# Performance work log

Hardware: AMD Instinct MI355X
Metric: run time of the kernel (lower is better)

The kernel has to match this reference:

```python
import jax, jax.numpy as jnp
import numpy as np

N, K, G = 4096, 4096, 128  # out_features, in_features, groupsize


def setup_inputs() -> dict:
    key = jax.random.key(0)
    k1, k2, k3, k4 = jax.random.split(key, 4)
    input = jax.random.normal(k1, (1, 2048, K), dtype=jnp.float32)
    # packed int4 weights: each byte holds two 4-bit codes (high nibble = even k, low = odd k)
    weight_packed = jax.random.randint(k2, (N, K // 2), 0, 256, dtype=jnp.int32)
    scales = jax.random.uniform(k3, (K // G, N), dtype=jnp.float32) * 0.02 + 1e-3
    zeros = jax.random.normal(k4, (K // G, N), dtype=jnp.float32) * 0.05
    scales_and_zeros = jnp.stack([scales, zeros], axis=-1)  # (K//G, N, 2)
    return {"input": input, "weight_packed": weight_packed,
            "scales_and_zeros": scales_and_zeros, "groupsize": G}


def reference(input, weight_packed, scales_and_zeros, groupsize):
    n, k_half = weight_packed.shape
    k = 2 * k_half
    g = k // groupsize
    # unpack two int4 codes per byte: high nibble first (even k index), then low nibble
    hi = (weight_packed >> 4) & 0xF
    lo = weight_packed & 0xF
    q = jnp.stack([hi, lo], axis=-1).reshape(n, k)  # (N, K), codes in [0,15]
    scales = scales_and_zeros[..., 0].T  # (N, G)
    zeros = scales_and_zeros[..., 1].T   # (N, G)
    # group-wise affine dequant: w = (q - 8) * scale + zero
    qg = q.reshape(n, g, groupsize).astype(jnp.float32)
    w = (qg - 8.0) * scales[:, :, None] + zeros[:, :, None]  # (N, G, gs)
    w = w.reshape(n, k)
    # out[..., n] = sum_k input[..., k] * w[n, k]
    return jnp.einsum('bsk,nk->bsn', input, w)
```

## Files before the change

### kernel.cpp

```cpp
#include <hip/hip_runtime.h>
#include <hip/hip_bf16.h>


using bf16x8 = __attribute__((ext_vector_type(8))) short;
using f32x16 = __attribute__((ext_vector_type(16))) float;

#define KK 4096
#define NN 4096
#define NT (KK / 64)

static __device__ __forceinline__ short f2bf(float f) {
    __hip_bfloat16 h = __float2bfloat16(f);
    return __builtin_bit_cast(short, h);
}

#define GLDS16(gptr, lptr) __builtin_amdgcn_global_load_lds( \
    (const __attribute__((address_space(1))) void*)(gptr),   \
    (__attribute__((address_space(3))) void*)(lptr), 16, 0, 0)

#define MFMA32 __builtin_amdgcn_mfma_f32_32x32x16_bf16

__global__ __launch_bounds__(256) void dequant_w(
    const int* __restrict__ W, const float* __restrict__ SZ,
    short* __restrict__ Wd)
{
    const int idx = blockIdx.x * 256 + threadIdx.x;
    const int n   = idx >> 9;
    const int q4  = idx & 511;
    const int kh0 = q4 << 2;
    const int g   = kh0 >> 6;
    const float2 sz = *(const float2*)(SZ + ((size_t)g * NN + n) * 2);
    const float scale = sz.x;
    const float zs    = sz.y - 8.0f * sz.x;
    int4 p = *(const int4*)(W + (size_t)n * (KK / 2) + kh0);
    int vals[4] = {p.x, p.y, p.z, p.w};
    bf16x8 r;
    #pragma unroll
    for (int j = 0; j < 4; ++j) {
        int v = vals[j];
        r[2 * j]     = f2bf((float)((v >> 4) & 0xF) * scale + zs);
        r[2 * j + 1] = f2bf((float)(v & 0xF) * scale + zs);
    }
    *(bf16x8*)&Wd[(size_t)n * KK + (kh0 << 1)] = r;
}

__global__ __launch_bounds__(256) void cvt_a(
    const float* __restrict__ A, short* __restrict__ Ab)
{
    const int idx = blockIdx.x * 256 + threadIdx.x;
    const float4* s = (const float4*)(A + (size_t)idx * 8);
    float4 u = s[0], v = s[1];
    bf16x8 r;
    r[0] = f2bf(u.x); r[1] = f2bf(u.y); r[2] = f2bf(u.z); r[3] = f2bf(u.w);
    r[4] = f2bf(v.x); r[5] = f2bf(v.y); r[6] = f2bf(v.z); r[7] = f2bf(v.w);
    *(bf16x8*)&Ab[(size_t)idx * 8] = r;
}

__global__ __launch_bounds__(512, 2) void gemm32(
    const short* __restrict__ Ab, const short* __restrict__ Bb,
    float* __restrict__ C)
{
    __shared__ short sA[3 * 256 * 64];
    __shared__ short sB[3 * 128 * 64];

    const int tid  = threadIdx.x;
    const int lane = tid & 63;
    const int wave = tid >> 6;
    const int wm   = wave >> 1;
    const int wn   = wave & 1;
    const int bm   = blockIdx.y * 256;
    const int bn   = blockIdx.x * 128;

    const int sl = lane >> 3;
    const int sc = (lane & 7) ^ sl;
    const short* aSt = Ab + (size_t)(bm + wave * 32 + sl) * KK + sc * 8;
    const short* bSt = Bb + (size_t)(bn + wave * 16 + sl) * KK + sc * 8;

    const int l31 = lane & 31;
    const int lx  = lane >> 5;
    const int l7  = lane & 7;
    const int px0 = ((0 + lx) ^ l7) * 8;
    const int px1 = ((2 + lx) ^ l7) * 8;
    const int px2 = ((4 + lx) ^ l7) * 8;
    const int px3 = ((6 + lx) ^ l7) * 8;
    const int aRd = (wm * 64 + l31) * 64;
    const int bRd = (wn * 64 + l31) * 64;

    f32x16 acc00 = {}, acc01 = {}, acc10 = {}, acc11 = {};

    #pragma unroll
    for (int l = 0; l < 4; ++l)
        GLDS16(aSt + (size_t)l * 8 * KK,      &sA[(wave * 32 + l * 8) * 64]);
    #pragma unroll
    for (int l = 0; l < 2; ++l)
        GLDS16(bSt + (size_t)l * 8 * KK,      &sB[(wave * 16 + l * 8) * 64]);
    #pragma unroll
    for (int l = 0; l < 4; ++l)
        GLDS16(aSt + (size_t)l * 8 * KK + 64, &sA[16384 + (wave * 32 + l * 8) * 64]);
    #pragma unroll
    for (int l = 0; l < 2; ++l)
        GLDS16(bSt + (size_t)l * 8 * KK + 64, &sB[8192 + (wave * 16 + l * 8) * 64]);
    asm volatile("s_waitcnt vmcnt(6)" ::: "memory");
    __builtin_amdgcn_s_barrier();

    int cur = 0;
    for (int t = 0; t < NT; ++t) {
        const int nxt = (cur == 0) ? 2 : cur - 1;
        const short* sAc = &sA[cur * 16384];
        const short* sBc = &sB[cur * 8192];
        short* sAn = &sA[nxt * 16384];
        short* sBn = &sB[nxt * 8192];
        const bool st = (t + 2 < NT);
        const int gk = (t + 2) * 64;

        {
            bf16x8 a00 = *(const bf16x8*)&sAc[aRd + px0];
            bf16x8 a01 = *(const bf16x8*)&sAc[aRd + px1];
            bf16x8 a10 = *(const bf16x8*)&sAc[aRd + 2048 + px0];
            bf16x8 a11 = *(const bf16x8*)&sAc[aRd + 2048 + px1];
            bf16x8 b00 = *(const bf16x8*)&sBc[bRd + px0];
            bf16x8 b01 = *(const bf16x8*)&sBc[bRd + px1];
            bf16x8 b10 = *(const bf16x8*)&sBc[bRd + 2048 + px0];
            bf16x8 b11 = *(const bf16x8*)&sBc[bRd + 2048 + px1];
            if (st) {
                GLDS16(aSt + (size_t)0 * 8 * KK + gk, sAn + (wave * 32 + 0) * 64);
                GLDS16(aSt + (size_t)1 * 8 * KK + gk, sAn + (wave * 32 + 8) * 64);
                GLDS16(bSt + (size_t)0 * 8 * KK + gk, sBn + (wave * 16 + 0) * 64);
            }
            __builtin_amdgcn_s_barrier();
            asm volatile("s_waitcnt lgkmcnt(0)" ::: "memory");
            __builtin_amdgcn_s_setprio(1);
            acc00 = MFMA32(a00, b00, acc00, 0, 0, 0);
            acc00 = MFMA32(a01, b01, acc00, 0, 0, 0);
            acc01 = MFMA32(a00, b10, acc01, 0, 0, 0);
            acc01 = MFMA32(a01, b11, acc01, 0, 0, 0);
            acc10 = MFMA32(a10, b00, acc10, 0, 0, 0);
            acc10 = MFMA32(a11, b01, acc10, 0, 0, 0);
            acc11 = MFMA32(a10, b10, acc11, 0, 0, 0);
            acc11 = MFMA32(a11, b11, acc11, 0, 0, 0);
            __builtin_amdgcn_s_setprio(0);
            __builtin_amdgcn_s_barrier();
        }

        {
            bf16x8 a00 = *(const bf16x8*)&sAc[aRd + px2];
            bf16x8 a01 = *(const bf16x8*)&sAc[aRd + px3];
            bf16x8 a10 = *(const bf16x8*)&sAc[aRd + 2048 + px2];
            bf16x8 a11 = *(const bf16x8*)&sAc[aRd + 2048 + px3];
            bf16x8 b00 = *(const bf16x8*)&sBc[bRd + px2];
            bf16x8 b01 = *(const bf16x8*)&sBc[bRd + px3];
            bf16x8 b10 = *(const bf16x8*)&sBc[bRd + 2048 + px2];
            bf16x8 b11 = *(const bf16x8*)&sBc[bRd + 2048 + px3];
            if (st) {
                GLDS16(aSt + (size_t)2 * 8 * KK + gk, sAn + (wave * 32 + 16) * 64);
                GLDS16(aSt + (size_t)3 * 8 * KK + gk, sAn + (wave * 32 + 24) * 64);
                GLDS16(bSt + (size_t)1 * 8 * KK + gk, sBn + (wave * 16 + 8) * 64);
            }
            __builtin_amdgcn_s_barrier();
            asm volatile("s_waitcnt lgkmcnt(0)" ::: "memory");
            __builtin_amdgcn_s_setprio(1);
            acc00 = MFMA32(a00, b00, acc00, 0, 0, 0);
            acc00 = MFMA32(a01, b01, acc00, 0, 0, 0);
            acc01 = MFMA32(a00, b10, acc01, 0, 0, 0);
            acc01 = MFMA32(a01, b11, acc01, 0, 0, 0);
            acc10 = MFMA32(a10, b00, acc10, 0, 0, 0);
            acc10 = MFMA32(a11, b01, acc10, 0, 0, 0);
            acc11 = MFMA32(a10, b10, acc11, 0, 0, 0);
            acc11 = MFMA32(a11, b11, acc11, 0, 0, 0);
            __builtin_amdgcn_s_setprio(0);
            if (t < NT - 2) {
                asm volatile("s_waitcnt vmcnt(6)" ::: "memory");
            } else {
                asm volatile("s_waitcnt vmcnt(0)" ::: "memory");
            }
            __builtin_amdgcn_s_barrier();
        }

        cur = (cur == 2) ? 0 : cur + 1;
    }

    {
        const int crow = lx * 4;
        float* Cp = C + (size_t)(bm + wm * 64) * NN + bn + wn * 64;
        #pragma unroll
        for (int m = 0; m < 2; ++m) {
            #pragma unroll
            for (int qr = 0; qr < 4; ++qr) {
                #pragma unroll
                for (int j = 0; j < 4; ++j) {
                    const int row = m * 32 + crow + j + 8 * qr;
                    float* dst = Cp + (size_t)row * NN + l31;
                    if (m == 0) {
                        dst[0]  = acc00[qr * 4 + j];
                        dst[32] = acc01[qr * 4 + j];
                    } else {
                        dst[0]  = acc10[qr * 4 + j];
                        dst[32] = acc11[qr * 4 + j];
                    }
                }
            }
        }
    }
}

using f32x4 = __attribute__((ext_vector_type(4))) float;
#define LDKF 72
__global__ __launch_bounds__(256) void wq4_gemm_fused(
    const float* __restrict__ A, const int* __restrict__ W,
    const float* __restrict__ SZ, float* __restrict__ C, int M)
{
    __shared__ short sA[128 * LDKF];
    __shared__ short sB[128 * LDKF];
    const int tid = threadIdx.x, lane = tid & 63, wave = tid >> 6;
    const int wr = (wave >> 1) << 6, wc = (wave & 1) << 6;
    const int bm = blockIdx.y * 128, bn = blockIdx.x * 128;
    const int ar = tid >> 2, ac = (tid & 3) << 4;
    const int br = tid >> 1, bh = (tid & 1) << 4;
    const float* Arow0 = A + (size_t)(bm + ar) * KK + ac;
    const float* Arow1 = A + (size_t)(bm + 64 + ar) * KK + ac;
    const int*   Wrow  = W + (size_t)(bn + br) * (KK / 2) + bh;
    const float* SZrow = SZ + (size_t)(bn + br) * 2;
    f32x4 acc[4][4] = {};
    for (int k0 = 0; k0 < KK; k0 += 64) {
        {
            const float4* s0 = (const float4*)(Arow0 + k0);
            const float4* s1 = (const float4*)(Arow1 + k0);
            float4 a0 = s0[0], a1 = s0[1], a2 = s0[2], a3 = s0[3];
            float4 b0 = s1[0], b1 = s1[1], b2 = s1[2], b3 = s1[3];
            auto cvt8 = [](float4 u, float4 v) -> bf16x8 {
                bf16x8 r;
                r[0] = f2bf(u.x); r[1] = f2bf(u.y); r[2] = f2bf(u.z); r[3] = f2bf(u.w);
                r[4] = f2bf(v.x); r[5] = f2bf(v.y); r[6] = f2bf(v.z); r[7] = f2bf(v.w);
                return r;
            };
            *(bf16x8*)&sA[ar * LDKF + ac]            = cvt8(a0, a1);
            *(bf16x8*)&sA[ar * LDKF + ac + 8]        = cvt8(a2, a3);
            *(bf16x8*)&sA[(64 + ar) * LDKF + ac]     = cvt8(b0, b1);
            *(bf16x8*)&sA[(64 + ar) * LDKF + ac + 8] = cvt8(b2, b3);
        }
        {
            const int g = k0 >> 7;
            const float2 sz = *(const float2*)(SZrow + (size_t)g * NN * 2);
            const float scale = sz.x, zs = sz.y - 8.0f * sz.x;
            const int4* src = (const int4*)(Wrow + (k0 >> 1));
            #pragma unroll
            for (int i = 0; i < 4; ++i) {
                int4 p = src[i];
                int vals[4] = {p.x, p.y, p.z, p.w};
                bf16x8 r;
                #pragma unroll
                for (int j = 0; j < 4; ++j) {
                    int v = vals[j];
                    r[2 * j]     = f2bf((float)((v >> 4) & 0xF) * scale + zs);
                    r[2 * j + 1] = f2bf((float)(v & 0xF) * scale + zs);
                }
                *(bf16x8*)&sB[br * LDKF + (bh << 1) + (i << 3)] = r;
            }
        }
        __syncthreads();
        #pragma unroll
        for (int ks = 0; ks < 2; ++ks) {
            const int col = (ks << 5) + ((lane >> 4) << 3);
            bf16x8 af[4], bfr[4];
            #pragma unroll
            for (int m = 0; m < 4; ++m)
                af[m] = *(const bf16x8*)&sA[(wr + m * 16 + (lane & 15)) * LDKF + col];
            #pragma unroll
            for (int n = 0; n < 4; ++n)
                bfr[n] = *(const bf16x8*)&sB[(wc + n * 16 + (lane & 15)) * LDKF + col];
            #pragma unroll
            for (int m = 0; m < 4; ++m)
                #pragma unroll
                for (int n = 0; n < 4; ++n)
                    acc[m][n] = __builtin_amdgcn_mfma_f32_16x16x32_bf16(
                        af[m], bfr[n], acc[m][n], 0, 0, 0);
        }
        __syncthreads();
    }
    float* Cp = C + (size_t)(bm + wr) * NN + bn + wc;
    const int cr = (lane >> 4) << 2, cc = lane & 15;
    #pragma unroll
    for (int m = 0; m < 4; ++m)
        #pragma unroll
        for (int j = 0; j < 4; ++j) {
            float* dst = Cp + (size_t)(m * 16 + cr + j) * NN + cc;
            #pragma unroll
            for (int n = 0; n < 4; ++n) dst[n * 16] = acc[m][n][j];
        }
}

extern "C" void kernel_launch(void* const* d_in, const int* in_sizes, int n_in,
                              void* d_out, int out_size, void* d_ws, size_t ws_size,
                              hipStream_t stream) {
    const float* A  = (const float*)d_in[0];
    const int*   W  = (const int*)d_in[1];
    const float* SZ = (const float*)d_in[2];
    float* C = (float*)d_out;

    const int M = in_sizes[0] / KK;

    const size_t wd_elems = (size_t)NN * KK;
    const size_t ab_elems = (size_t)M * KK;
    const size_t need = (wd_elems + ab_elems) * sizeof(short);

    if (ws_size >= need && (M % 256) == 0) {
        short* Wd = (short*)d_ws;
        short* Ab = Wd + wd_elems;
        dequant_w<<<NN * (KK / 8) / 256, 256, 0, stream>>>(W, SZ, Wd);
        cvt_a<<<(int)(ab_elems / 8 / 256), 256, 0, stream>>>(A, Ab);
        dim3 grid(NN / 128, M / 256);
        gemm32<<<grid, dim3(512), 0, stream>>>(Ab, Wd, C);
    } else {
        dim3 grid(NN / 128, M / 128);
        wq4_gemm_fused<<<grid, dim3(256), 0, stream>>>(A, W, SZ, C, M);
    }
}
```

Measured before the change: 102.7 us.

## Software-pipeline LDS fragment reads with MFMA using register double buffering

Restructures the GEMM main loop so the LDS reads for the next half-tile go into a second register set while MFMAs run on the current one. It prefetches the first half of the next K tile after the barrier and cuts the per-iteration barriers from four to one. The aim is to hide LDS read latency behind MFMA issue. In exchange it raises VGPR pressure, which matters at 2 blocks per CU, and the single barrier plus relaxed vmcnt(3) waits put ordering of the triple-buffered stages at risk.

```diff
diff --git a/kernel.cpp b/kernel.cpp
--- a/kernel.cpp
+++ b/kernel.cpp
@@ -56,7 +56,7 @@
     *(bf16x8*)&Ab[(size_t)idx * 8] = r;
 }
 
-__global__ __launch_bounds__(512, 2) void gemm32(
+__global__ __launch_bounds__(512, 2) void gemm_pl(
     const short* __restrict__ Ab, const short* __restrict__ Bb,
     float* __restrict__ C)
 {
@@ -87,6 +87,8 @@
     const int bRd = (wn * 64 + l31) * 64;
 
     f32x16 acc00 = {}, acc01 = {}, acc10 = {}, acc11 = {};
+    bf16x8 pA00, pA01, pA10, pA11, pB00, pB01, pB10, pB11;
+    bf16x8 qA00, qA01, qA10, qA11, qB00, qB01, qB10, qB11;
 
     #pragma unroll
     for (int l = 0; l < 4; ++l)
@@ -103,80 +105,97 @@
     asm volatile("s_waitcnt vmcnt(6)" ::: "memory");
     __builtin_amdgcn_s_barrier();
 
+    pA00 = *(const bf16x8*)&sA[aRd + px0];
+    pA01 = *(const bf16x8*)&sA[aRd + px1];
+    pA10 = *(const bf16x8*)&sA[aRd + 2048 + px0];
+    pA11 = *(const bf16x8*)&sA[aRd + 2048 + px1];
+    pB00 = *(const bf16x8*)&sB[bRd + px0];
+    pB01 = *(const bf16x8*)&sB[bRd + px1];
+    pB10 = *(const bf16x8*)&sB[bRd + 2048 + px0];
+    pB11 = *(const bf16x8*)&sB[bRd + 2048 + px1];
+    asm volatile("s_waitcnt lgkmcnt(0)" ::: "memory");
+    __builtin_amdgcn_sched_barrier(0);
+
     int cur = 0;
     for (int t = 0; t < NT; ++t) {
-        const int nxt = (cur == 0) ? 2 : cur - 1;
+        const int nxt1 = (cur == 2) ? 0 : cur + 1;
+        const int nxt2 = (nxt1 == 2) ? 0 : nxt1 + 1;
         const short* sAc = &sA[cur * 16384];
         const short* sBc = &sB[cur * 8192];
-        short* sAn = &sA[nxt * 16384];
-        short* sBn = &sB[nxt * 8192];
+        const short* sA1 = &sA[nxt1 * 16384];
+        const short* sB1 = &sB[nxt1 * 8192];
+        short* sAn = &sA[nxt2 * 16384];
+        short* sBn = &sB[nxt2 * 8192];
         const bool st = (t + 2 < NT);
         const int gk = (t + 2) * 64;
 
-        {
-            bf16x8 a00 = *(const bf16x8*)&sAc[aRd + px0];
-            bf16x8 a01 = *(const bf16x8*)&sAc[aRd + px1];
-            bf16x8 a10 = *(const bf16x8*)&sAc[aRd + 2048 + px0];
-            bf16x8 a11 = *(const bf16x8*)&sAc[aRd + 2048 + px1];
-            bf16x8 b00 = *(const bf16x8*)&sBc[bRd + px0];
-            bf16x8 b01 = *(const bf16x8*)&sBc[bRd + px1];
-            bf16x8 b10 = *(const bf16x8*)&sBc[bRd + 2048 + px0];
-            bf16x8 b11 = *(const bf16x8*)&sBc[bRd + 2048 + px1];
-            if (st) {
-                GLDS16(aSt + (size_t)0 * 8 * KK + gk, sAn + (wave * 32 + 0) * 64);
-                GLDS16(aSt + (size_t)1 * 8 * KK + gk, sAn + (wave * 32 + 8) * 64);
-                GLDS16(bSt + (size_t)0 * 8 * KK + gk, sBn + (wave * 16 + 0) * 64);
-            }
-            __builtin_amdgcn_s_barrier();
-            asm volatile("s_waitcnt lgkmcnt(0)" ::: "memory");
-            __builtin_amdgcn_s_setprio(1);
-            acc00 = MFMA32(a00, b00, acc00, 0, 0, 0);
-            acc00 = MFMA32(a01, b01, acc00, 0, 0, 0);
-            acc01 = MFMA32(a00, b10, acc01, 0, 0, 0);
-            acc01 = MFMA32(a01, b11, acc01, 0, 0, 0);
-            acc10 = MFMA32(a10, b00, acc10, 0, 0, 0);
-            acc10 = MFMA32(a11, b01, acc10, 0, 0, 0);
-            acc11 = MFMA32(a10, b10, acc11, 0, 0, 0);
-            acc11 = MFMA32(a11, b11, acc11, 0, 0, 0);
-            __builtin_amdgcn_s_setprio(0);
-            __builtin_amdgcn_s_barrier();
-        }
-
-        {
-            bf16x8 a00 = *(const bf16x8*)&sAc[aRd + px2];
-            bf16x8 a01 = *(const bf16x8*)&sAc[aRd + px3];
-            bf16x8 a10 = *(const bf16x8*)&sAc[aRd + 2048 + px2];
-            bf16x8 a11 = *(const bf16x8*)&sAc[aRd + 2048 + px3];
-            bf16x8 b00 = *(const bf16x8*)&sBc[bRd + px2];
-            bf16x8 b01 = *(const bf16x8*)&sBc[bRd + px3];
-            bf16x8 b10 = *(const bf16x8*)&sBc[bRd + 2048 + px2];
-            bf16x8 b11 = *(const bf16x8*)&sBc[bRd + 2048 + px3];
-            if (st) {
-                GLDS16(aSt + (size_t)2 * 8 * KK + gk, sAn + (wave * 32 + 16) * 64);
-                GLDS16(aSt + (size_t)3 * 8 * KK + gk, sAn + (wave * 32 + 24) * 64);
-                GLDS16(bSt + (size_t)1 * 8 * KK + gk, sBn + (wave * 16 + 8) * 64);
-            }
-            __builtin_amdgcn_s_barrier();
-            asm volatile("s_waitcnt lgkmcnt(0)" ::: "memory");
-            __builtin_amdgcn_s_setprio(1);
-            acc00 = MFMA32(a00, b00, acc00, 0, 0, 0);
-            acc00 = MFMA32(a01, b01, acc00, 0, 0, 0);
-            acc01 = MFMA32(a00, b10, acc01, 0, 0, 0);
-            acc01 = MFMA32(a01, b11, acc01, 0, 0, 0);
-            acc10 = MFMA32(a10, b00, acc10, 0, 0, 0);
-            acc10 = MFMA32(a11, b01, acc10, 0, 0, 0);
-            acc11 = MFMA32(a10, b10, acc11, 0, 0, 0);
-            acc11 = MFMA32(a11, b11, acc11, 0, 0, 0);
-            __builtin_amdgcn_s_setprio(0);
-            if (t < NT - 2) {
-                asm volatile("s_waitcnt vmcnt(6)" ::: "memory");
-            } else {
-                asm volatile("s_waitcnt vmcnt(0)" ::: "memory");
-            }
-            __builtin_amdgcn_s_barrier();
-        }
-
-        cur = (cur == 2) ? 0 : cur + 1;
+        qA00 = *(const bf16x8*)&sAc[aRd + px2];
+        qA01 = *(const bf16x8*)&sAc[aRd + px3];
+        qA10 = *(const bf16x8*)&sAc[aRd + 2048 + px2];
+        qA11 = *(const bf16x8*)&sAc[aRd + 2048 + px3];
+        qB00 = *(const bf16x8*)&sBc[bRd + px2];
+        qB01 = *(const bf16x8*)&sBc[bRd + px3];
+        qB10 = *(const bf16x8*)&sBc[bRd + 2048 + px2];
+        qB11 = *(const bf16x8*)&sBc[bRd + 2048 + px3];
+        if (st) {
+            GLDS16(aSt + (size_t)0 * 8 * KK + gk, sAn + (wave * 32 + 0) * 64);
+            GLDS16(aSt + (size_t)1 * 8 * KK + gk, sAn + (wave * 32 + 8) * 64);
+            GLDS16(bSt + (size_t)0 * 8 * KK + gk, sBn + (wave * 16 + 0) * 64);
+        }
+        __builtin_amdgcn_sched_barrier(0);
+
+        __builtin_amdgcn_s_setprio(1);
+        acc00 = MFMA32(pA00, pB00, acc00, 0, 0, 0);
+        acc00 = MFMA32(pA01, pB01, acc00, 0, 0, 0);
+        acc01 = MFMA32(pA00, pB10, acc01, 0, 0, 0);
+        acc01 = MFMA32(pA01, pB11, acc01, 0, 0, 0);
+        acc10 = MFMA32(pA10, pB00, acc10, 0, 0, 0);
+        acc10 = MFMA32(pA11, pB01, acc10, 0, 0, 0);
+        acc11 = MFMA32(pA10, pB10, acc11, 0, 0, 0);
+        acc11 = MFMA32(pA11, pB11, acc11, 0, 0, 0);
+        __builtin_amdgcn_s_setprio(0);
+
+        asm volatile("s_waitcnt lgkmcnt(0)" ::: "memory");
+        __builtin_amdgcn_sched_barrier(0);
+        if (t < NT - 2) {
+            asm volatile("s_waitcnt vmcnt(3)" ::: "memory");
+        } else {
+            asm volatile("s_waitcnt vmcnt(0)" ::: "memory");
+        }
+        __builtin_amdgcn_s_barrier();
+
+        if (t + 1 < NT) {
+            pA00 = *(const bf16x8*)&sA1[aRd + px0];
+            pA01 = *(const bf16x8*)&sA1[aRd + px1];
+            pA10 = *(const bf16x8*)&sA1[aRd + 2048 + px0];
+            pA11 = *(const bf16x8*)&sA1[aRd + 2048 + px1];
+            pB00 = *(const bf16x8*)&sB1[bRd + px0];
+            pB01 = *(const bf16x8*)&sB1[bRd + px1];
+            pB10 = *(const bf16x8*)&sB1[bRd + 2048 + px0];
+            pB11 = *(const bf16x8*)&sB1[bRd + 2048 + px1];
+        }
+        if (st) {
+            GLDS16(aSt + (size_t)2 * 8 * KK + gk, sAn + (wave * 32 + 16) * 64);
+            GLDS16(aSt + (size_t)3 * 8 * KK + gk, sAn + (wave * 32 + 24) * 64);
+            GLDS16(bSt + (size_t)1 * 8 * KK + gk, sBn + (wave * 16 + 8) * 64);
+        }
+        __builtin_amdgcn_sched_barrier(0);
+
+        __builtin_amdgcn_s_setprio(1);
+        acc00 = MFMA32(qA00, qB00, acc00, 0, 0, 0);
+        acc00 = MFMA32(qA01, qB01, acc00, 0, 0, 0);
+        acc01 = MFMA32(qA00, qB10, acc01, 0, 0, 0);
+        acc01 = MFMA32(qA01, qB11, acc01, 0, 0, 0);
+        acc10 = MFMA32(qA10, qB00, acc10, 0, 0, 0);
+        acc10 = MFMA32(qA11, qB01, acc10, 0, 0, 0);
+        acc11 = MFMA32(qA10, qB10, acc11, 0, 0, 0);
+        acc11 = MFMA32(qA11, qB11, acc11, 0, 0, 0);
+        __builtin_amdgcn_s_setprio(0);
+
+        asm volatile("s_waitcnt lgkmcnt(0)" ::: "memory");
+        __builtin_amdgcn_sched_barrier(0);
+
+        cur = nxt1;
     }
 
     {
@@ -309,7 +328,7 @@
         dequant_w<<<NN * (KK / 8) / 256, 256, 0, stream>>>(W, SZ, Wd);
         cvt_a<<<(int)(ab_elems / 8 / 256), 256, 0, stream>>>(A, Ab);
         dim3 grid(NN / 128, M / 256);
-        gemm32<<<grid, dim3(512), 0, stream>>>(Ab, Wd, C);
+        gemm_pl<<<grid, dim3(512), 0, stream>>>(Ab, Wd, C);
     } else {
         dim3 grid(NN / 128, M / 128);
         wq4_gemm_fused<<<grid, dim3(256), 0, stream>>>(A, W, SZ, C, M);
```

Result: faster. 93.78 us (-8.7%).
